# Kernel tuning notes

Measured on AMD Instinct MI355X. Metric: run time of the kernel, lower is better.

## Reference

```python
import jax, jax.numpy as jnp
from jax import lax
import numpy as np

DIM = 256


def setup_inputs() -> dict:
    key = jax.random.key(0)
    ks = jax.random.split(key, 7)
    B, C, H, W = 16, DIM, 64, 64
    s = 0.02
    return {
        "x": jax.random.normal(ks[0], (B, C, H, W), dtype=jnp.float32),
        "qkv_w": jax.random.normal(ks[1], (3 * C, C), dtype=jnp.float32) * s,
        "qkv_b": jnp.zeros((3 * C,), dtype=jnp.float32),
        "proj_w": jax.random.normal(ks[2], (C, C), dtype=jnp.float32) * s,
        "proj_b": jnp.zeros((C,), dtype=jnp.float32),
        "conv_w": jax.random.normal(ks[3], (C, C, 3, 3), dtype=jnp.float32) * s,
        "conv_b": jnp.zeros((C,), dtype=jnp.float32),
    }


def reference(x, qkv_w, qkv_b, proj_w, proj_b, conv_w, conv_b):
    B, C, H, W = x.shape
    N = H * W
    scale = C ** (-0.5)
    # qkv on channels-last tokens: [B,N,3C]
    xp = x.transpose(0, 2, 3, 1).reshape(B, N, C)
    qkv = xp @ qkv_w.T + qkv_b
    q, k, v = jnp.split(qkv, 3, axis=-1)  # each [B,N,C]
    q = q.transpose(0, 2, 1)  # [B,C,N]
    v = v.transpose(0, 2, 1)  # [B,C,N]
    # channel attention: [B,C,C]
    attn = jax.nn.softmax(jnp.einsum('bcn,bnd->bcd', q, k) * scale, axis=-1)
    out = jnp.einsum('bcd,bdn->bcn', attn, v).transpose(0, 2, 1)  # [B,N,C]
    out = out @ proj_w.T + proj_b  # [B,N,C]
    # faithful to original: direct reshape [B,N,C] -> [B,C,H,W]
    attn_out = out.reshape(B, C, H, W)
    conv_out = lax.conv_general_dilated(
        x, conv_w, window_strides=(1, 1), padding=[(1, 1), (1, 1)],
        dimension_numbers=('NCHW', 'OIHW', 'NCHW'))
    conv_out = conv_out + conv_b[None, :, None, None]
    return attn_out + conv_out
```

## Files before the change

### kernel.cpp

```cpp
#include <hip/hip_runtime.h>
#include <hip/hip_bf16.h>

typedef unsigned short u16;
typedef __bf16 bf16x8 __attribute__((ext_vector_type(8)));
typedef float f32x4 __attribute__((ext_vector_type(4)));

#define BATCH 16
#define C 256
#define NTOK 4096
#define CN 1048576

__device__ __forceinline__ u16 f2b(float f) {
  __hip_bfloat16 h = __float2bfloat16(f);
  return __builtin_bit_cast(u16, h);
}
__device__ __forceinline__ float b2f(u16 u) {
  unsigned int x = ((unsigned int)u) << 16;
  return __builtin_bit_cast(float, x);
}

__device__ __forceinline__ void glds16(const u16* g, u16* l) {
  __builtin_amdgcn_global_load_lds(
      (const __attribute__((address_space(1))) unsigned int*)(g),
      (__attribute__((address_space(3))) unsigned int*)(l), 16, 0, 0);
}

__global__ __launch_bounds__(256) void prep_x_kernel(
    const float* __restrict__ x, u16* __restrict__ xbf, u16* __restrict__ xT,
    float* __restrict__ rws) {
  __shared__ float t[32][33];
  int b = blockIdx.z;
  int c0 = blockIdx.y * 32, n0 = blockIdx.x * 32;
  int tid = threadIdx.x;
  int i = tid >> 3, j4 = (tid & 7) * 4;
  const float* xb = x + (long)b * CN;
  float4 v = *(const float4*)(xb + (long)(c0 + i) * NTOK + n0 + j4);
  ushort4 bv;
  bv.x = f2b(v.x); bv.y = f2b(v.y); bv.z = f2b(v.z); bv.w = f2b(v.w);
  *(ushort4*)(xbf + (long)b * CN + (long)(c0 + i) * NTOK + n0 + j4) = bv;
  t[i][j4 + 0] = v.x; t[i][j4 + 1] = v.y; t[i][j4 + 2] = v.z; t[i][j4 + 3] = v.w;
  __syncthreads();
  ushort4 o;
  o.x = f2b(t[j4 + 0][i]); o.y = f2b(t[j4 + 1][i]);
  o.z = f2b(t[j4 + 2][i]); o.w = f2b(t[j4 + 3][i]);
  *(ushort4*)(xT + (long)b * CN + (long)(n0 + i) * C + c0 + j4) = o;
  if (tid < 32) {
    float s = 0.f;
#pragma unroll
    for (int j = 0; j < 32; ++j) s += t[tid][j];
    atomicAdd(&rws[b * C + c0 + tid], s);
  }
}

__global__ __launch_bounds__(256) void prep_w_kernel(
    const float* __restrict__ qkv_w, const float* __restrict__ proj_w,
    const float* __restrict__ conv_w, u16* __restrict__ WqT, u16* __restrict__ Wk,
    u16* __restrict__ WvT, u16* __restrict__ Pw, u16* __restrict__ cw,
    float* __restrict__ rws, u16* __restrict__ zbuf) {
  int idx = blockIdx.x * 256 + threadIdx.x;
  if (idx < 4096) rws[idx] = 0.f;
  if (idx < 256) zbuf[idx] = 0;
  if (idx < 65536) {
    WqT[(idx & 255) * 256 + (idx >> 8)] = f2b(qkv_w[idx]);
  } else if (idx < 131072) {
    int e = idx - 65536;
    Wk[e] = f2b(qkv_w[65536 + e]);
  } else if (idx < 196608) {
    int e = idx - 131072;
    int i = e >> 8, d = e & 255;
    WvT[e] = f2b(qkv_w[131072 + d * 256 + i]);
  } else if (idx < 262144) {
    int e = idx - 196608;
    Pw[e] = f2b(proj_w[e]);
  } else if (idx < 851968) {
    int e = idx - 262144;
    int o = e / 2304;
    int rem = e - o * 2304;
    int tap = rem >> 8, i = rem & 255;
    cw[e] = f2b(conv_w[o * 2304 + i * 9 + tap]);
  }
}

template <int EPI>
__global__ __launch_bounds__(256, 2) void gemm_glds_kernel(
    const u16* __restrict__ A, const u16* __restrict__ B, void* __restrict__ Cv,
    int K, int lda, int ldb, int ldc, int tilesN, long sA, long sB, long sC,
    float scale, const float* __restrict__ e1, const float* __restrict__ e2,
    const float* __restrict__ e3, const float* __restrict__ e4, int e34stride) {
  int b = blockIdx.z, ks = blockIdx.y;
  A += (long)b * sA + (long)ks * K;
  B += (long)b * sB + (long)ks * K;
  int ty = blockIdx.x / tilesN, tx = blockIdx.x % tilesN;
  int row0 = ty * 128, col0 = tx * 128;

  __shared__ u16 lA[2][4096];
  __shared__ u16 lB[2][4096];

  int tid = threadIdx.x;
  int lane = tid & 63, wv = tid >> 6;
  int wm = wv >> 1, wn = wv & 1;
  int fr = lane & 15, kq = lane >> 4;
  int kqs = kq ^ ((fr >> 1) & 3);

  int c0 = wv * 128 + lane, c1 = c0 + 64;
  int r0s = c0 >> 2, r1s = c1 >> 2;
  int ls0 = (c0 & 3) ^ ((r0s >> 1) & 3);
  int ls1 = (c1 & 3) ^ ((r1s >> 1) & 3);
  const u16* pA0 = A + (long)(row0 + r0s) * lda + ls0 * 8;
  const u16* pA1 = A + (long)(row0 + r1s) * lda + ls1 * 8;
  const u16* pB0 = B + (long)(col0 + r0s) * ldb + ls0 * 8;
  const u16* pB1 = B + (long)(col0 + r1s) * ldb + ls1 * 8;
  int dst0 = wv * 1024, dst1 = wv * 1024 + 512;

  f32x4 acc[4][4] = {};

  auto STAGE = [&](int buf, int t) {
    int k0 = t << 5;
    glds16(pA0 + k0, &lA[buf][dst0]);
    glds16(pA1 + k0, &lA[buf][dst1]);
    glds16(pB0 + k0, &lB[buf][dst0]);
    glds16(pB1 + k0, &lB[buf][dst1]);
  };
  auto COMPUTE = [&](int buf) {
    bf16x8 af[4], bfr[4];
#pragma unroll
    for (int m = 0; m < 4; ++m)
      af[m] = *(const bf16x8*)&lA[buf][(wm * 64 + m * 16 + fr) * 32 + kqs * 8];
#pragma unroll
    for (int n = 0; n < 4; ++n)
      bfr[n] = *(const bf16x8*)&lB[buf][(wn * 64 + n * 16 + fr) * 32 + kqs * 8];
#pragma unroll
    for (int m = 0; m < 4; ++m)
#pragma unroll
      for (int n = 0; n < 4; ++n)
        acc[m][n] = __builtin_amdgcn_mfma_f32_16x16x32_bf16(af[m], bfr[n], acc[m][n], 0, 0, 0);
  };

  int nk = K >> 5, cur = 0;
  STAGE(0, 0);
  __syncthreads();
  for (int t = 0; t < nk; ++t) {
    if (t + 1 < nk) STAGE(cur ^ 1, t + 1);
    COMPUTE(cur);
    __syncthreads();
    cur ^= 1;
  }

  if (EPI == 5) {
    __hip_bfloat16* Cb =
        (__hip_bfloat16*)Cv + ((long)b * gridDim.y + ks) * sC;
#pragma unroll
    for (int m = 0; m < 4; ++m)
#pragma unroll
      for (int n = 0; n < 4; ++n)
#pragma unroll
        for (int r = 0; r < 4; ++r) {
          int gr = row0 + wm * 64 + m * 16 + kq * 4 + r;
          int gc = col0 + wn * 64 + n * 16 + fr;
          Cb[(long)gr * ldc + gc] = __float2bfloat16(acc[m][n][r]);
        }
  }
}

template <int EPI>
__global__ __launch_bounds__(256, 2) void gemm64_kernel(
    const u16* __restrict__ A, const u16* __restrict__ B, void* __restrict__ Cv,
    long sA, long sB, long sC, float scale, const float* __restrict__ e1,
    const float* __restrict__ e2, const float* __restrict__ e3,
    const float* __restrict__ e4, int e34stride) {
  if (EPI == 4 && blockIdx.x == 16) {
    int bb = blockIdx.z, j = threadIdx.x;
    const u16* m = A + (long)bb * sA + (long)j * 256;
    float s = 0.f;
    for (int d = 0; d < 256; ++d) s += b2f(m[d]) * e1[512 + d];
    float* cbout = const_cast<float*>(e4);
    cbout[bb * 256 + j] = e2[j] + s;
    return;
  }
  int b = blockIdx.z;
  A += (long)b * sA;
  B += (long)b * sB;
  int ty = blockIdx.x >> 2, tx = blockIdx.x & 3;
  int row0 = ty * 64, col0 = tx * 64;

  __shared__ u16 lA[2][2048];
  __shared__ u16 lB[2][2048];

  int tid = threadIdx.x;
  int lane = tid & 63, w = tid >> 6;
  int wm = w >> 1, wn = w & 1;
  int fr = lane & 15, kq = lane >> 4;
  int kqs = kq ^ ((fr >> 1) & 3);

  int rs = tid >> 2;
  int ls = (tid & 3) ^ ((rs >> 1) & 3);
  const u16* pA = A + (long)(row0 + rs) * 256 + ls * 8;
  const u16* pB = B + (long)(col0 + rs) * 256 + ls * 8;
  int dst = w * 512;

  f32x4 acc[2][2] = {};

  auto STAGE = [&](int buf, int t) {
    int k0 = t << 5;
    glds16(pA + k0, &lA[buf][dst]);
    glds16(pB + k0, &lB[buf][dst]);
  };
  auto COMPUTE = [&](int buf) {
    bf16x8 af[2], bfr[2];
#pragma unroll
    for (int m = 0; m < 2; ++m)
      af[m] = *(const bf16x8*)&lA[buf][(wm * 32 + m * 16 + fr) * 32 + kqs * 8];
#pragma unroll
    for (int n = 0; n < 2; ++n)
      bfr[n] = *(const bf16x8*)&lB[buf][(wn * 32 + n * 16 + fr) * 32 + kqs * 8];
#pragma unroll
    for (int m = 0; m < 2; ++m)
#pragma unroll
      for (int n = 0; n < 2; ++n)
        acc[m][n] = __builtin_amdgcn_mfma_f32_16x16x32_bf16(af[m], bfr[n], acc[m][n], 0, 0, 0);
  };

  int cur = 0;
  STAGE(0, 0);
  __syncthreads();
  for (int t = 0; t < 8; ++t) {
    if (t + 1 < 8) STAGE(cur ^ 1, t + 1);
    COMPUTE(cur);
    __syncthreads();
    cur ^= 1;
  }

  if (EPI == 1 || EPI == 4) {
    __hip_bfloat16* Cb = (__hip_bfloat16*)Cv + (long)b * sC;
#pragma unroll
    for (int m = 0; m < 2; ++m)
#pragma unroll
      for (int n = 0; n < 2; ++n)
#pragma unroll
        for (int r = 0; r < 4; ++r) {
          int gr = row0 + wm * 32 + m * 16 + kq * 4 + r;
          int gc = col0 + wn * 32 + n * 16 + fr;
          Cb[(long)gr * 256 + gc] = __float2bfloat16(acc[m][n][r]);
        }
  } else if (EPI == 2) {
    float* Cb = (float*)Cv + (long)b * sC;
    const float* ub = e3 + (long)b * e34stride;
    const float* wb = e4 + (long)b * e34stride;
#pragma unroll
    for (int m = 0; m < 2; ++m)
#pragma unroll
      for (int n = 0; n < 2; ++n)
#pragma unroll
        for (int r = 0; r < 4; ++r) {
          int gr = row0 + wm * 32 + m * 16 + kq * 4 + r;
          int gc = col0 + wn * 32 + n * 16 + fr;
          float v = acc[m][n][r] + e1[gr] * ub[gc] + e2[gc] * wb[gr] +
                    4096.0f * e1[gr] * e2[gc];
          Cb[(long)gr * 256 + gc] = v * scale;
        }
  }
}

__global__ __launch_bounds__(256) void reduceG_T1_bias_kernel(
    const u16* __restrict__ Gp, const u16* __restrict__ WqT,
    u16* __restrict__ T1, const float* __restrict__ qkv_w,
    const float* __restrict__ r, float* __restrict__ u, float* __restrict__ w) {
  int b = blockIdx.y;
  if (blockIdx.x < 64) {
    __shared__ float g[4][256];
    int tid = threadIdx.x;
    int e = blockIdx.x * 1024 + tid * 4;
    const u16* base = Gp + (long)b * 8 * 65536;
    float s0 = 0.f, s1 = 0.f, s2 = 0.f, s3 = 0.f;
#pragma unroll
    for (int sl = 0; sl < 8; ++sl) {
      ushort4 v = *(const ushort4*)(base + (long)sl * 65536 + e);
      s0 += b2f(v.x); s1 += b2f(v.y); s2 += b2f(v.z); s3 += b2f(v.w);
    }
    int rr = tid >> 6, cc = (tid & 63) * 4;
    g[rr][cc + 0] = s0; g[rr][cc + 1] = s1;
    g[rr][cc + 2] = s2; g[rr][cc + 3] = s3;
    __syncthreads();
    int c = tid;
    float a0 = 0.f, a1 = 0.f, a2 = 0.f, a3 = 0.f;
#pragma unroll 4
    for (int i = 0; i < 256; ++i) {
      float wq = b2f(WqT[i * 256 + c]);
      a0 += wq * g[0][i]; a1 += wq * g[1][i];
      a2 += wq * g[2][i]; a3 += wq * g[3][i];
    }
    ushort4 o;
    o.x = f2b(a0); o.y = f2b(a1); o.z = f2b(a2); o.w = f2b(a3);
    *(ushort4*)(T1 + (long)b * 65536 + (long)c * 256 + blockIdx.x * 4) = o;
  } else {
    int t = threadIdx.x;
    const float* rb = r + b * C;
    float su = 0.f, sw = 0.f;
    for (int i = 0; i < C; ++i) {
      float rv = rb[i];
      su += qkv_w[(256 + t) * 256 + i] * rv;
      sw += qkv_w[t * 256 + i] * rv;
    }
    u[b * C + t] = su;
    w[b * C + t] = sw;
  }
}

__global__ __launch_bounds__(256) void softmax_kernel(const float* __restrict__ S,
                                                      u16* __restrict__ attnT) {
  int row = blockIdx.x;
  int t = threadIdx.x;
  float v = S[(long)row * C + t];
  __shared__ float red[256];
  red[t] = v; __syncthreads();
  for (int st = 128; st > 0; st >>= 1) {
    if (t < st) red[t] = fmaxf(red[t], red[t + st]);
    __syncthreads();
  }
  float mx = red[0];
  __syncthreads();
  float e = __expf(v - mx);
  red[t] = e; __syncthreads();
  for (int st = 128; st > 0; st >>= 1) {
    if (t < st) red[t] += red[t + st];
    __syncthreads();
  }
  float inv = 1.0f / red[0];
  int b = row >> 8, c = row & 255;
  attnT[(long)b * 65536 + t * 256 + c] = f2b(e * inv);
}

__global__ __launch_bounds__(256, 2) void convattn_kernel(
    const u16* __restrict__ xT, const u16* __restrict__ cw,
    const u16* __restrict__ W2, const u16* __restrict__ zbuf,
    const float* __restrict__ conv_b, const float* __restrict__ cb,
    float* __restrict__ out) {
  int b = blockIdx.y;
  int to = blockIdx.x >> 5;
  int tn = blockIdx.x & 31;
  int row0 = to * 128, col0 = tn * 128;
  const u16* xTb = xT + (long)b * CN;
  const u16* W2b = W2 + (long)b * 65536;

  __shared__ u16 lA[2][8192];
  __shared__ u16 lB[2][8192];

  int tid = threadIdx.x;
  int lane = tid & 63, w = tid >> 6;
  int wm = w >> 1, wn = w & 1;
  int fr = lane & 15, kq = lane >> 4;
  int fx = fr & 7;

  int lr = lane >> 3, sl = lane & 7;
  int ss = sl ^ lr;

  const u16* aA[4]; const u16* pBt[4]; int hh[4], ww[4];
  const u16* zsrc = zbuf + ss * 8;
#pragma unroll
  for (int i = 0; i < 4; ++i) {
    int r = w * 32 + i * 8 + lr;
    aA[i] = cw + (long)(row0 + r) * 2304 + ss * 8;
    int t = col0 + r;
    hh[i] = t >> 6; ww[i] = t & 63;
    pBt[i] = xTb + (long)t * 256 + ss * 8;
  }
  int nb = col0 >> 8, jb = col0 & 255;

  f32x4 acc[4][4] = {};
  const u16 *at0, *at1, *at2, *at3, *bt0, *bt1, *bt2, *bt3;

  auto set_tap = [&](int tap) {
    int dh = tap / 3 - 1, dw = tap % 3 - 1;
    long sh = (long)(dh * 64 + dw) * 256;
    at0 = aA[0] + tap * 256; at1 = aA[1] + tap * 256;
    at2 = aA[2] + tap * 256; at3 = aA[3] + tap * 256;
    bool v0 = ((unsigned)(hh[0] + dh) < 64u) && ((unsigned)(ww[0] + dw) < 64u);
    bool v1 = ((unsigned)(hh[1] + dh) < 64u) && ((unsigned)(ww[1] + dw) < 64u);
    bool v2 = ((unsigned)(hh[2] + dh) < 64u) && ((unsigned)(ww[2] + dw) < 64u);
    bool v3 = ((unsigned)(hh[3] + dh) < 64u) && ((unsigned)(ww[3] + dw) < 64u);
    bt0 = v0 ? pBt[0] + sh : zsrc;
    bt1 = v1 ? pBt[1] + sh : zsrc;
    bt2 = v2 ? pBt[2] + sh : zsrc;
    bt3 = v3 ? pBt[3] + sh : zsrc;
  };
  auto set_attn = [&]() {
#pragma unroll
    for (int i = 0; i < 4; ++i) {
      int r = w * 32 + i * 8 + lr;
      const u16* a = xTb + (long)((row0 + r) * 16 + nb) * 256 + ss * 8;
      const u16* bb = W2b + (long)(jb + r) * 256 + ss * 8;
      if (i == 0) { at0 = a; bt0 = bb; }
      else if (i == 1) { at1 = a; bt1 = bb; }
      else if (i == 2) { at2 = a; bt2 = bb; }
      else { at3 = a; bt3 = bb; }
    }
  };

  auto STAGE = [&](int buf, int chunk) {
    int k = chunk * 64;
    glds16(at0 + k, &lA[buf][(w * 32 + 0) * 64]);
    glds16(at1 + k, &lA[buf][(w * 32 + 8) * 64]);
    glds16(at2 + k, &lA[buf][(w * 32 + 16) * 64]);
    glds16(at3 + k, &lA[buf][(w * 32 + 24) * 64]);
    glds16(bt0 + k, &lB[buf][(w * 32 + 0) * 64]);
    glds16(bt1 + k, &lB[buf][(w * 32 + 8) * 64]);
    glds16(bt2 + k, &lB[buf][(w * 32 + 16) * 64]);
    glds16(bt3 + k, &lB[buf][(w * 32 + 24) * 64]);
  };
  auto COMPUTE = [&](int buf) {
    bf16x8 af[4][2], bf[4][2];
#pragma unroll
    for (int m = 0; m < 4; ++m) {
      int row = wm * 64 + m * 16 + fr;
#pragma unroll
      for (int kh = 0; kh < 2; ++kh)
        af[m][kh] = *(const bf16x8*)&lA[buf][row * 64 + (((kh << 2) + kq) ^ fx) * 8];
    }
#pragma unroll
    for (int n = 0; n < 4; ++n) {
      int row = wn * 64 + n * 16 + fr;
#pragma unroll
      for (int kh = 0; kh < 2; ++kh)
        bf[n][kh] = *(const bf16x8*)&lB[buf][row * 64 + (((kh << 2) + kq) ^ fx) * 8];
    }
    __builtin_amdgcn_s_setprio(1);
#pragma unroll
    for (int kh = 0; kh < 2; ++kh)
#pragma unroll
      for (int m = 0; m < 4; ++m)
#pragma unroll
        for (int n = 0; n < 4; ++n)
          acc[m][n] = __builtin_amdgcn_mfma_f32_16x16x32_bf16(af[m][kh], bf[n][kh], acc[m][n], 0, 0, 0);
    __builtin_amdgcn_s_setprio(0);
  };

  set_tap(0);
  STAGE(0, 0);
  asm volatile("s_waitcnt vmcnt(0)" ::: "memory");
  __builtin_amdgcn_sched_barrier(0);
  __builtin_amdgcn_s_barrier();
  __builtin_amdgcn_sched_barrier(0);

  int buf = 0;
#pragma unroll 1
  for (int T = 0; T < 10; ++T) {
#pragma unroll
    for (int j = 0; j < 4; ++j) {
      if (!(T == 9 && j == 3)) {
        if (j < 3) {
          STAGE(buf ^ 1, j + 1);
        } else {
          if (T < 8) set_tap(T + 1);
          else set_attn();
          STAGE(buf ^ 1, 0);
        }
      }
      COMPUTE(buf);
      asm volatile("s_waitcnt vmcnt(0)" ::: "memory");
      __builtin_amdgcn_sched_barrier(0);
      __builtin_amdgcn_s_barrier();
      __builtin_amdgcn_sched_barrier(0);
      buf ^= 1;
    }
  }

  float* ob = out + (long)b * CN;
  const float* cbb = cb + b * C;
#pragma unroll
  for (int m = 0; m < 4; ++m) {
    int go = row0 + wm * 64 + m * 16 + kq * 4;
#pragma unroll
    for (int nn = 0; nn < 4; ++nn) {
      int cc = wn * 64 + nn * 16 + fr;
      float cbv = cbb[jb + cc];
#pragma unroll
      for (int r = 0; r < 4; ++r)
        ob[(long)(go + r) * NTOK + col0 + cc] =
            acc[m][nn][r] + conv_b[go + r] + cbv;
    }
  }
}

extern "C" void kernel_launch(void* const* d_in, const int* in_sizes, int n_in,
                              void* d_out, int out_size, void* d_ws, size_t ws_size,
                              hipStream_t stream) {
  const float* x = (const float*)d_in[0];
  const float* qkv_w = (const float*)d_in[1];
  const float* qkv_b = (const float*)d_in[2];
  const float* proj_w = (const float*)d_in[3];
  const float* proj_b = (const float*)d_in[4];
  const float* conv_w = (const float*)d_in[5];
  const float* conv_b = (const float*)d_in[6];
  float* out = (float*)d_out;
  char* ws = (char*)d_ws;

  u16* xbf = (u16*)(ws);
  u16* xT = (u16*)(ws + 33554432);
  u16* T1bf = (u16*)(ws + 67108864);
  u16* Gpart = (u16*)(ws + 69206016);
  float* Sf = (float*)(ws + 71303168);
  u16* attnT = (u16*)(ws + 75497472);
  u16* Mbf = (u16*)(ws + 77594624);
  u16* W2bf = (u16*)(ws + 79691776);
  u16* WqT = (u16*)(ws + 85983232);
  u16* Wk = (u16*)(ws + 86114304);
  u16* WvT = (u16*)(ws + 86245376);
  u16* Pw = (u16*)(ws + 86376448);
  u16* cw = (u16*)(ws + 86507520);
  float* rws = (float*)(ws + 87687168);
  float* uws = (float*)(ws + 87703552);
  float* wws = (float*)(ws + 87719936);
  float* cb = (float*)(ws + 87736320);
  u16* zbuf = (u16*)(ws + 87752704);

  prep_w_kernel<<<3328, 256, 0, stream>>>(qkv_w, proj_w, conv_w, WqT, Wk, WvT,
                                          Pw, cw, rws, zbuf);
  prep_x_kernel<<<dim3(128, 8, BATCH), 256, 0, stream>>>(x, xbf, xT, rws);

  gemm_glds_kernel<5><<<dim3(4, 8, BATCH), 256, 0, stream>>>(
      xbf, xbf, Gpart, 512, 4096, 4096, 256, 2, CN, CN, 65536,
      0.f, nullptr, nullptr, nullptr, nullptr, 0);
  reduceG_T1_bias_kernel<<<dim3(65, BATCH), 256, 0, stream>>>(
      Gpart, WqT, T1bf, qkv_w, rws, uws, wws);

  gemm64_kernel<2><<<dim3(16, 1, BATCH), 256, 0, stream>>>(
      T1bf, Wk, Sf, 65536, 0, 65536,
      0.0625f, qkv_b, qkv_b + 256, uws, wws, 256);

  softmax_kernel<<<BATCH * C, 256, 0, stream>>>(Sf, attnT);

  gemm64_kernel<1><<<dim3(16, 1, BATCH), 256, 0, stream>>>(
      Pw, attnT, Mbf, 0, 65536, 65536,
      0.f, nullptr, nullptr, nullptr, nullptr, 0);
  gemm64_kernel<4><<<dim3(17, 1, BATCH), 256, 0, stream>>>(
      Mbf, WvT, W2bf, 65536, 0, 65536,
      0.f, qkv_b, proj_b, nullptr, cb, 256);

  convattn_kernel<<<dim3(64, BATCH), 256, 0, stream>>>(xT, cw, W2bf, zbuf,
                                                       conv_b, cb, out);
}
```

Before: 207.0 us.

## Fuse score GEMM with softmax and merge prep kernels into one launch

```diff
diff --git a/kernel.cpp b/kernel.cpp
--- a/kernel.cpp
+++ b/kernel.cpp
@@ -25,68 +25,65 @@
       (__attribute__((address_space(3))) unsigned int*)(l), 16, 0, 0);
 }
 
-__global__ __launch_bounds__(256) void prep_x_kernel(
-    const float* __restrict__ x, u16* __restrict__ xbf, u16* __restrict__ xT,
-    float* __restrict__ rws) {
+__global__ __launch_bounds__(256) void prep_kernel(
+    const float* __restrict__ x, const float* __restrict__ qkv_w,
+    const float* __restrict__ proj_w, const float* __restrict__ conv_w,
+    u16* __restrict__ xbf, u16* __restrict__ xT, float* __restrict__ rws,
+    u16* __restrict__ WqT, u16* __restrict__ Wk, u16* __restrict__ WvT,
+    u16* __restrict__ Pw, u16* __restrict__ cw) {
   __shared__ float t[32][33];
-  int b = blockIdx.z;
-  int c0 = blockIdx.y * 32, n0 = blockIdx.x * 32;
+  int bx = blockIdx.x;
   int tid = threadIdx.x;
-  int i = tid >> 3, j4 = (tid & 7) * 4;
-  const float* xb = x + (long)b * CN;
-  float4 v = *(const float4*)(xb + (long)(c0 + i) * NTOK + n0 + j4);
-  ushort4 bv;
-  bv.x = f2b(v.x); bv.y = f2b(v.y); bv.z = f2b(v.z); bv.w = f2b(v.w);
-  *(ushort4*)(xbf + (long)b * CN + (long)(c0 + i) * NTOK + n0 + j4) = bv;
-  t[i][j4 + 0] = v.x; t[i][j4 + 1] = v.y; t[i][j4 + 2] = v.z; t[i][j4 + 3] = v.w;
-  __syncthreads();
-  ushort4 o;
-  o.x = f2b(t[j4 + 0][i]); o.y = f2b(t[j4 + 1][i]);
-  o.z = f2b(t[j4 + 2][i]); o.w = f2b(t[j4 + 3][i]);
-  *(ushort4*)(xT + (long)b * CN + (long)(n0 + i) * C + c0 + j4) = o;
-  if (tid < 32) {
-    float s = 0.f;
-#pragma unroll
-    for (int j = 0; j < 32; ++j) s += t[tid][j];
-    atomicAdd(&rws[b * C + c0 + tid], s);
-  }
-}
-
-__global__ __launch_bounds__(256) void prep_w_kernel(
-    const float* __restrict__ qkv_w, const float* __restrict__ proj_w,
-    const float* __restrict__ conv_w, u16* __restrict__ WqT, u16* __restrict__ Wk,
-    u16* __restrict__ WvT, u16* __restrict__ Pw, u16* __restrict__ cw,
-    float* __restrict__ rws, u16* __restrict__ zbuf) {
-  int idx = blockIdx.x * 256 + threadIdx.x;
-  if (idx < 4096) rws[idx] = 0.f;
-  if (idx < 256) zbuf[idx] = 0;
-  if (idx < 65536) {
-    WqT[(idx & 255) * 256 + (idx >> 8)] = f2b(qkv_w[idx]);
-  } else if (idx < 131072) {
-    int e = idx - 65536;
-    Wk[e] = f2b(qkv_w[65536 + e]);
-  } else if (idx < 196608) {
-    int e = idx - 131072;
-    int i = e >> 8, d = e & 255;
-    WvT[e] = f2b(qkv_w[131072 + d * 256 + i]);
-  } else if (idx < 262144) {
-    int e = idx - 196608;
-    Pw[e] = f2b(proj_w[e]);
-  } else if (idx < 851968) {
-    int e = idx - 262144;
-    int o = e / 2304;
-    int rem = e - o * 2304;
-    int tap = rem >> 8, i = rem & 255;
-    cw[e] = f2b(conv_w[o * 2304 + i * 9 + tap]);
+  if (bx < 16384) {
+    int n0 = (bx & 127) * 32;
+    int c0 = ((bx >> 7) & 7) * 32;
+    int b = bx >> 10;
+    int i = tid >> 3, j4 = (tid & 7) * 4;
+    const float* xb = x + (long)b * CN;
+    float4 v = *(const float4*)(xb + (long)(c0 + i) * NTOK + n0 + j4);
+    ushort4 bv;
+    bv.x = f2b(v.x); bv.y = f2b(v.y); bv.z = f2b(v.z); bv.w = f2b(v.w);
+    *(ushort4*)(xbf + (long)b * CN + (long)(c0 + i) * NTOK + n0 + j4) = bv;
+    t[i][j4 + 0] = v.x; t[i][j4 + 1] = v.y; t[i][j4 + 2] = v.z; t[i][j4 + 3] = v.w;
+    __syncthreads();
+    ushort4 o;
+    o.x = f2b(t[j4 + 0][i]); o.y = f2b(t[j4 + 1][i]);
+    o.z = f2b(t[j4 + 2][i]); o.w = f2b(t[j4 + 3][i]);
+    *(ushort4*)(xT + (long)b * CN + (long)(n0 + i) * C + c0 + j4) = o;
+    if (tid < 32) {
+      float s = 0.f;
+#pragma unroll
+      for (int j = 0; j < 32; ++j) s += t[tid][j];
+      atomicAdd(&rws[b * C + c0 + tid], s);
+    }
+  } else {
+    int idx = (bx - 16384) * 256 + tid;
+    if (idx < 65536) {
+      WqT[(idx & 255) * 256 + (idx >> 8)] = f2b(qkv_w[idx]);
+    } else if (idx < 131072) {
+      int e = idx - 65536;
+      Wk[e] = f2b(qkv_w[65536 + e]);
+    } else if (idx < 196608) {
+      int e = idx - 131072;
+      int i = e >> 8, d = e & 255;
+      WvT[e] = f2b(qkv_w[131072 + d * 256 + i]);
+    } else if (idx < 262144) {
+      int e = idx - 196608;
+      Pw[e] = f2b(proj_w[e]);
+    } else if (idx < 851968) {
+      int e = idx - 262144;
+      int o = e / 2304;
+      int rem = e - o * 2304;
+      int tap = rem >> 8, i = rem & 255;
+      cw[e] = f2b(conv_w[o * 2304 + i * 9 + tap]);
+    }
   }
 }
 
 template <int EPI>
 __global__ __launch_bounds__(256, 2) void gemm_glds_kernel(
     const u16* __restrict__ A, const u16* __restrict__ B, void* __restrict__ Cv,
-    int K, int lda, int ldb, int ldc, int tilesN, long sA, long sB, long sC,
-    float scale, const float* __restrict__ e1, const float* __restrict__ e2,
-    const float* __restrict__ e3, const float* __restrict__ e4, int e34stride) {
+    int K, int lda, int ldb, int ldc, int tilesN, long sA, long sB, long sC) {
   int b = blockIdx.z, ks = blockIdx.y;
   A += (long)b * sA + (long)ks * K;
   B += (long)b * sB + (long)ks * K;
@@ -165,9 +162,8 @@
 template <int EPI>
 __global__ __launch_bounds__(256, 2) void gemm64_kernel(
     const u16* __restrict__ A, const u16* __restrict__ B, void* __restrict__ Cv,
-    long sA, long sB, long sC, float scale, const float* __restrict__ e1,
-    const float* __restrict__ e2, const float* __restrict__ e3,
-    const float* __restrict__ e4, int e34stride) {
+    long sA, long sB, long sC, const float* __restrict__ e1,
+    const float* __restrict__ e2, const float* __restrict__ e4) {
   if (EPI == 4 && blockIdx.x == 16) {
     int bb = blockIdx.z, j = threadIdx.x;
     const u16* m = A + (long)bb * sA + (long)j * 256;
@@ -230,35 +226,129 @@
     cur ^= 1;
   }
 
-  if (EPI == 1 || EPI == 4) {
-    __hip_bfloat16* Cb = (__hip_bfloat16*)Cv + (long)b * sC;
+  __hip_bfloat16* Cb = (__hip_bfloat16*)Cv + (long)b * sC;
+#pragma unroll
+  for (int m = 0; m < 2; ++m)
+#pragma unroll
+    for (int n = 0; n < 2; ++n)
+#pragma unroll
+      for (int r = 0; r < 4; ++r) {
+        int gr = row0 + wm * 32 + m * 16 + kq * 4 + r;
+        int gc = col0 + wn * 32 + n * 16 + fr;
+        Cb[(long)gr * 256 + gc] = __float2bfloat16(acc[m][n][r]);
+      }
+}
+
+__global__ __launch_bounds__(256, 2) void s_softmax_kernel(
+    const u16* __restrict__ T1, const u16* __restrict__ Wk,
+    u16* __restrict__ attnT, const float* __restrict__ qkv_b,
+    const float* __restrict__ uws, const float* __restrict__ wws) {
+  int b = blockIdx.y;
+  int r0 = blockIdx.x * 32;
+  const u16* Ab = T1 + (long)b * 65536 + (long)r0 * 256;
+
+  __shared__ u16 lA[2][1024];
+  __shared__ u16 lB[2][8192];
+  __shared__ float sf[32][257];
+  __shared__ float red[32][8];
+  __shared__ float rmax[32], rinv[32];
+
+  int tid = threadIdx.x;
+  int lane = tid & 63, w = tid >> 6;
+  int fr = lane & 15, kq = lane >> 4;
+  int kqs = kq ^ ((fr >> 1) & 3);
+
+  int rsA = tid >> 2;
+  int lsA = (tid & 3) ^ ((rsA >> 1) & 3);
+  const u16* pA = Ab + (long)rsA * 256 + lsA * 8;
+  int lrB = lane >> 2;
+  int lsB = (lane & 3) ^ ((lrB >> 1) & 3);
+  const u16* pB = Wk + (long)(w * 64 + lrB) * 256 + lsB * 8;
+
+  f32x4 acc[2][4] = {};
+
+  auto STAGE = [&](int buf, int t) {
+    int k0 = t << 5;
+    if (w == 0) glds16(pA + k0, &lA[buf][0]);
+    if (w == 1) glds16(pA + k0, &lA[buf][512]);
+    glds16(pB + k0, &lB[buf][(w * 64 + 0) * 32]);
+    glds16(pB + 16 * 256 + k0, &lB[buf][(w * 64 + 16) * 32]);
+    glds16(pB + 32 * 256 + k0, &lB[buf][(w * 64 + 32) * 32]);
+    glds16(pB + 48 * 256 + k0, &lB[buf][(w * 64 + 48) * 32]);
+  };
+  auto COMPUTE = [&](int buf) {
+    bf16x8 af[2], bfr[4];
 #pragma unroll
     for (int m = 0; m < 2; ++m)
-#pragma unroll
-      for (int n = 0; n < 2; ++n)
-#pragma unroll
-        for (int r = 0; r < 4; ++r) {
-          int gr = row0 + wm * 32 + m * 16 + kq * 4 + r;
-          int gc = col0 + wn * 32 + n * 16 + fr;
-          Cb[(long)gr * 256 + gc] = __float2bfloat16(acc[m][n][r]);
-        }
-  } else if (EPI == 2) {
-    float* Cb = (float*)Cv + (long)b * sC;
-    const float* ub = e3 + (long)b * e34stride;
-    const float* wb = e4 + (long)b * e34stride;
+      af[m] = *(const bf16x8*)&lA[buf][(m * 16 + fr) * 32 + kqs * 8];
+#pragma unroll
+    for (int n = 0; n < 4; ++n)
+      bfr[n] = *(const bf16x8*)&lB[buf][(w * 64 + n * 16 + fr) * 32 + kqs * 8];
 #pragma unroll
     for (int m = 0; m < 2; ++m)
 #pragma unroll
-      for (int n = 0; n < 2; ++n)
-#pragma unroll
-        for (int r = 0; r < 4; ++r) {
-          int gr = row0 + wm * 32 + m * 16 + kq * 4 + r;
-          int gc = col0 + wn * 32 + n * 16 + fr;
-          float v = acc[m][n][r] + e1[gr] * ub[gc] + e2[gc] * wb[gr] +
-                    4096.0f * e1[gr] * e2[gc];
-          Cb[(long)gr * 256 + gc] = v * scale;
-        }
-  }
+      for (int n = 0; n < 4; ++n)
+        acc[m][n] = __builtin_amdgcn_mfma_f32_16x16x32_bf16(af[m], bfr[n], acc[m][n], 0, 0, 0);
+  };
+
+  int cur = 0;
+  STAGE(0, 0);
+  __syncthreads();
+  for (int t = 0; t < 8; ++t) {
+    if (t + 1 < 8) STAGE(cur ^ 1, t + 1);
+    COMPUTE(cur);
+    __syncthreads();
+    cur ^= 1;
+  }
+
+  const float* ub = uws + b * 256;
+  const float* wb = wws + b * 256;
+#pragma unroll
+  for (int m = 0; m < 2; ++m)
+#pragma unroll
+    for (int n = 0; n < 4; ++n)
+#pragma unroll
+      for (int r = 0; r < 4; ++r) {
+        int row = m * 16 + kq * 4 + r;
+        int col = w * 64 + n * 16 + fr;
+        float qb = qkv_b[r0 + row];
+        float v = acc[m][n][r] + qb * ub[col] + qkv_b[256 + col] * wb[r0 + row] +
+                  4096.0f * qb * qkv_b[256 + col];
+        sf[row][col] = v * 0.0625f;
+      }
+  __syncthreads();
+
+  int rr = tid >> 3, sg = (tid & 7) * 32;
+  float mx = -3.4e38f;
+  for (int c2 = sg; c2 < sg + 32; ++c2) mx = fmaxf(mx, sf[rr][c2]);
+  red[rr][tid & 7] = mx;
+  __syncthreads();
+  if (tid < 32) {
+    float m2 = red[tid][0];
+#pragma unroll
+    for (int k = 1; k < 8; ++k) m2 = fmaxf(m2, red[tid][k]);
+    rmax[tid] = m2;
+  }
+  __syncthreads();
+  float m2 = rmax[rr], sm = 0.f;
+  for (int c2 = sg; c2 < sg + 32; ++c2) {
+    float e = __expf(sf[rr][c2] - m2);
+    sf[rr][c2] = e;
+    sm += e;
+  }
+  red[rr][tid & 7] = sm;
+  __syncthreads();
+  if (tid < 32) {
+    float s2 = red[tid][0];
+#pragma unroll
+    for (int k = 1; k < 8; ++k) s2 += red[tid][k];
+    rinv[tid] = 1.0f / s2;
+  }
+  __syncthreads();
+  int c = tid;
+  u16* aT = attnT + (long)b * 65536 + (long)c * 256 + r0;
+#pragma unroll 8
+  for (int r = 0; r < 32; ++r) aT[r] = f2b(sf[r][c] * rinv[r]);
 }
 
 __global__ __launch_bounds__(256) void reduceG_T1_bias_kernel(
@@ -304,30 +394,6 @@
     u[b * C + t] = su;
     w[b * C + t] = sw;
   }
-}
-
-__global__ __launch_bounds__(256) void softmax_kernel(const float* __restrict__ S,
-                                                      u16* __restrict__ attnT) {
-  int row = blockIdx.x;
-  int t = threadIdx.x;
-  float v = S[(long)row * C + t];
-  __shared__ float red[256];
-  red[t] = v; __syncthreads();
-  for (int st = 128; st > 0; st >>= 1) {
-    if (t < st) red[t] = fmaxf(red[t], red[t + st]);
-    __syncthreads();
-  }
-  float mx = red[0];
-  __syncthreads();
-  float e = __expf(v - mx);
-  red[t] = e; __syncthreads();
-  for (int st = 128; st > 0; st >>= 1) {
-    if (t < st) red[t] += red[t + st];
-    __syncthreads();
-  }
-  float inv = 1.0f / red[0];
-  int b = row >> 8, c = row & 255;
-  attnT[(long)b * 65536 + t * 256 + c] = f2b(e * inv);
 }
 
 __global__ __launch_bounds__(256, 2) void convattn_kernel(
@@ -498,7 +564,6 @@
   u16* xT = (u16*)(ws + 33554432);
   u16* T1bf = (u16*)(ws + 67108864);
   u16* Gpart = (u16*)(ws + 69206016);
-  float* Sf = (float*)(ws + 71303168);
   u16* attnT = (u16*)(ws + 75497472);
   u16* Mbf = (u16*)(ws + 77594624);
   u16* W2bf = (u16*)(ws + 79691776);
@@ -508,33 +573,28 @@
   u16* Pw = (u16*)(ws + 86376448);
   u16* cw = (u16*)(ws + 86507520);
   float* rws = (float*)(ws + 87687168);
-  float* uws = (float*)(ws + 87703552);
-  float* wws = (float*)(ws + 87719936);
-  float* cb = (float*)(ws + 87736320);
-  u16* zbuf = (u16*)(ws + 87752704);
-
-  prep_w_kernel<<<3328, 256, 0, stream>>>(qkv_w, proj_w, conv_w, WqT, Wk, WvT,
-                                          Pw, cw, rws, zbuf);
-  prep_x_kernel<<<dim3(128, 8, BATCH), 256, 0, stream>>>(x, xbf, xT, rws);
+  u16* zbuf = (u16*)(ws + 87703552);
+  float* uws = (float*)(ws + 87704064);
+  float* wws = (float*)(ws + 87720448);
+  float* cb = (float*)(ws + 87736832);
+
+  hipMemsetAsync(ws + 87687168, 0, 16896, stream);
+
+  prep_kernel<<<19712, 256, 0, stream>>>(x, qkv_w, proj_w, conv_w, xbf, xT,
+                                         rws, WqT, Wk, WvT, Pw, cw);
 
   gemm_glds_kernel<5><<<dim3(4, 8, BATCH), 256, 0, stream>>>(
-      xbf, xbf, Gpart, 512, 4096, 4096, 256, 2, CN, CN, 65536,
-      0.f, nullptr, nullptr, nullptr, nullptr, 0);
+      xbf, xbf, Gpart, 512, 4096, 4096, 256, 2, CN, CN, 65536);
   reduceG_T1_bias_kernel<<<dim3(65, BATCH), 256, 0, stream>>>(
       Gpart, WqT, T1bf, qkv_w, rws, uws, wws);
 
-  gemm64_kernel<2><<<dim3(16, 1, BATCH), 256, 0, stream>>>(
-      T1bf, Wk, Sf, 65536, 0, 65536,
-      0.0625f, qkv_b, qkv_b + 256, uws, wws, 256);
-
-  softmax_kernel<<<BATCH * C, 256, 0, stream>>>(Sf, attnT);
+  s_softmax_kernel<<<dim3(8, BATCH), 256, 0, stream>>>(
+      T1bf, Wk, attnT, qkv_b, uws, wws);
 
   gemm64_kernel<1><<<dim3(16, 1, BATCH), 256, 0, stream>>>(
-      Pw, attnT, Mbf, 0, 65536, 65536,
-      0.f, nullptr, nullptr, nullptr, nullptr, 0);
+      Pw, attnT, Mbf, 0, 65536, 65536, nullptr, nullptr, nullptr);
   gemm64_kernel<4><<<dim3(17, 1, BATCH), 256, 0, stream>>>(
-      Mbf, WvT, W2bf, 65536, 0, 65536,
-      0.f, qkv_b, proj_b, nullptr, cb, 256);
+      Mbf, WvT, W2bf, 65536, 0, 65536, qkv_b, proj_b, cb);
 
   convattn_kernel<<<dim3(64, BATCH), 256, 0, stream>>>(xT, cw, W2bf, zbuf,
                                                        conv_b, cb, out);
```

Result: no change. 204.5 us (-1.2%).
